# Kernel optimization log

Measured on AMD Instinct MI355X. Metric: run time of the kernel, lower is better.

The kernel has to match this reference:

```python
import jax, jax.numpy as jnp
import numpy as np

IN_C, OUT_C, K, STRIDE, PAD = 128, 256, 3, 1, 1
B, H, W = 32, 56, 56


def setup_inputs() -> dict:
    key = jax.random.key(0)
    kx, kw = jax.random.split(key)
    x = jax.random.normal(kx, (B, IN_C, H, W), dtype=jnp.float32)
    # He init, matching torch.randn(out_c,in_c,k,k) * (2/(in_c*k*k))**0.5
    Wk = jax.random.normal(kw, (OUT_C, IN_C, K, K), dtype=jnp.float32) * (2.0 / (IN_C * K * K)) ** 0.5
    b = jnp.zeros((OUT_C,), dtype=jnp.float32)
    return {"x": x, "Wk": Wk, "b": b}


def reference(x, Wk, b):
    # Same math as the module's zero-pad + im2col + GEMM pipeline,
    # expressed as a direct convolution (implicit GEMM).
    out = jax.lax.conv_general_dilated(
        x, Wk,
        window_strides=(STRIDE, STRIDE),
        padding=[(PAD, PAD), (PAD, PAD)],
        dimension_numbers=("NCHW", "OIHW", "NCHW"),
    )
    return out + b[None, :, None, None]
```

## Files before the change

kernel.cpp:

```cpp
#include <hip/hip_runtime.h>
#include <hip/hip_bf16.h>

#define IN_C  128
#define OUT_C 256
#define HIMG  56
#define WIMG  56
#define BIMG  32
#define HW    (HIMG * WIMG)
#define KW    1152

#define BM    128
#define TH    4
#define NLOC  224
#define XROWS 6
#define XCOLS 58
#define NPIXT (XROWS * XCOLS)
#define LDK   40

typedef __attribute__((ext_vector_type(8))) short short8;
typedef __attribute__((ext_vector_type(4))) float float4_;

__device__ __forceinline__ unsigned short f32_to_bf16_rne(float f) {
    unsigned u = __builtin_bit_cast(unsigned, f);
    u += 0x7FFFu + ((u >> 16) & 1u);
    return (unsigned short)(u >> 16);
}

__global__ void repack_w(const float* __restrict__ Wk, unsigned short* __restrict__ Wt) {
    int idx = blockIdx.x * 256 + threadIdx.x;
    if (idx >= OUT_C * KW) return;
    int oc  = idx / KW;
    int rem = idx - oc * KW;
    int r   = rem >> 7;
    int ic  = rem & 127;
    Wt[idx] = f32_to_bf16_rne(Wk[oc * KW + ic * 9 + r]);
}

__global__ __launch_bounds__(256, 2) void conv_gemm(
    const float* __restrict__ x, const unsigned short* __restrict__ Wt,
    const float* __restrict__ bias, float* __restrict__ out)
{
    __shared__ short As[BM * LDK];
    __shared__ short Xs[NPIXT * 32];

    const int tid  = threadIdx.x;
    const int lane = tid & 63;
    const int wid  = tid >> 6;
    const int bx   = blockIdx.x;
    const int b    = bx / 14;
    const int h0   = (bx - b * 14) * TH;
    const int oc0  = blockIdx.y * BM;

    const int wm = (wid >> 1) * 64;
    const int wn = (wid & 1) * 112;

    int lp0[7], outoff[7];
    #pragma unroll
    for (int ni = 0; ni < 7; ++ni) {
        int nl  = wn + ni * 16 + (lane & 15);
        int ht_ = nl / 56;
        int wt_ = nl - ht_ * 56;
        lp0[ni]    = (ht_ + 1) * XCOLS + (wt_ + 1);
        outoff[ni] = (h0 + ht_) * WIMG + wt_;
    }

    const short* aptr[4];
    #pragma unroll
    for (int mi = 0; mi < 4; ++mi)
        aptr[mi] = &As[(wm + mi * 16 + (lane & 15)) * LDK + (lane >> 4) * 8];

    float4_ acc[4][7];
    #pragma unroll
    for (int mi = 0; mi < 4; ++mi)
        #pragma unroll
        for (int ni = 0; ni < 7; ++ni) acc[mi][ni] = (float4_)0.0f;

    const int am = tid >> 1, ako = (tid & 1) * 16;
    const int q  = lane >> 4;

    short8 w0, w1;
    {
        const unsigned short* srcA = Wt + (size_t)(oc0 + am) * KW + 0 * 128 + 0 * 32 + ako;
        w0 = *(const short8*)srcA;
        w1 = *(const short8*)(srcA + 8);
    }

    for (int t = 0; t < 36; ++t) {
        const int icq = t / 9;
        const int r   = t - icq * 9;

        if (r == 0) {
            for (int pix = tid; pix < NPIXT; pix += 256) {
                int row  = pix / XCOLS;
                int colw = pix - row * XCOLS;
                int h = h0 + row - 1;
                int w = colw - 1;
                bool valid = ((unsigned)h < HIMG) & ((unsigned)w < WIMG);
                const int sw = (pix >> 1) & 3;
                #pragma unroll
                for (int qb = 0; qb < 4; ++qb) {
                    const float* src = x + (size_t)(b * IN_C + icq * 32 + qb * 8) * HW
                                         + (ptrdiff_t)(h * WIMG + w);
                    short8 v;
                    #pragma unroll
                    for (int j = 0; j < 8; ++j) {
                        float f = valid ? src[(size_t)j * HW] : 0.0f;
                        v[j] = (short)f32_to_bf16_rne(f);
                    }
                    *(short8*)&Xs[pix * 32 + (qb ^ sw) * 8] = v;
                }
            }
        }

        *(short8*)&As[am * LDK + ako]     = w0;
        *(short8*)&As[am * LDK + ako + 8] = w1;
        if (t < 35) {
            const int t1   = t + 1;
            const int icq1 = t1 / 9;
            const int r1   = t1 - icq1 * 9;
            const unsigned short* srcA =
                Wt + (size_t)(oc0 + am) * KW + r1 * 128 + icq1 * 32 + ako;
            w0 = *(const short8*)srcA;
            w1 = *(const short8*)(srcA + 8);
        }
        __syncthreads();

        const int doff = (r / 3 - 1) * XCOLS + (r - (r / 3) * 3 - 1);
        short8 afr[4], bfr[7];
        #pragma unroll
        for (int mi = 0; mi < 4; ++mi) afr[mi] = *(const short8*)aptr[mi];
        #pragma unroll
        for (int ni = 0; ni < 7; ++ni) {
            int lp   = lp0[ni] + doff;
            int slot = q ^ ((lp >> 1) & 3);
            bfr[ni]  = *(const short8*)&Xs[lp * 32 + slot * 8];
        }
        #pragma unroll
        for (int mi = 0; mi < 4; ++mi)
            #pragma unroll
            for (int ni = 0; ni < 7; ++ni)
                acc[mi][ni] = __builtin_amdgcn_mfma_f32_16x16x32_bf16(
                    afr[mi], bfr[ni], acc[mi][ni], 0, 0, 0);
        __syncthreads();
    }

    const int rowg = (lane >> 4) * 4;
    #pragma unroll
    for (int mi = 0; mi < 4; ++mi) {
        #pragma unroll
        for (int v = 0; v < 4; ++v) {
            const int oc = oc0 + wm + mi * 16 + rowg + v;
            const float bv = bias[oc];
            float* obase = out + (size_t)(b * OUT_C + oc) * HW;
            #pragma unroll
            for (int ni = 0; ni < 7; ++ni)
                obase[outoff[ni]] = acc[mi][ni][v] + bv;
        }
    }
}

extern "C" void kernel_launch(void* const* d_in, const int* in_sizes, int n_in,
                              void* d_out, int out_size, void* d_ws, size_t ws_size,
                              hipStream_t stream) {
    const float* x    = (const float*)d_in[0];
    const float* Wk   = (const float*)d_in[1];
    const float* bias = (const float*)d_in[2];
    float* out        = (float*)d_out;
    unsigned short* Wt = (unsigned short*)d_ws;

    repack_w<<<dim3((OUT_C * KW + 255) / 256), dim3(256), 0, stream>>>(Wk, Wt);
    conv_gemm<<<dim3(BIMG * (HIMG / TH), OUT_C / BM), dim3(256), 0, stream>>>(x, Wt, bias, out);
}
```

Measured before the change: 214.6 us.

## Pre-pack input to padded NHWC bf16 and async-pipeline LDS tiles

Adds a pre-pass that converts x into a zero-padded NHWC bf16 buffer and repacks the weights into pre-swizzled per-step tiles. The GEMM kernel then fills LDS directly with global_load_lds async copies: a 4-deep ring buffer for weight tiles and a double buffer for input tiles. It waits with manual vmcnt counts and a single barrier per step, and raises wave priority around the MFMA block. This removes the in-kernel strided fp32 gathers, conversions and the second barrier. It costs an extra transpose kernel, extra workspace traffic and more LDS, which may reduce occupancy.

Result: faster. 201.1 us (-6.3%).

```diff
diff --git a/kernel.cpp b/kernel.cpp
--- a/kernel.cpp
+++ b/kernel.cpp
@@ -1,5 +1,4 @@
 #include <hip/hip_runtime.h>
-#include <hip/hip_bf16.h>
 
 #define IN_C  128
 #define OUT_C 256
@@ -11,11 +10,16 @@
 
 #define BM    128
 #define TH    4
-#define NLOC  224
 #define XROWS 6
 #define XCOLS 58
 #define NPIXT (XROWS * XCOLS)
-#define LDK   40
+#define XS_SH (NPIXT * 32)
+#define AS_SH 4096
+#define NT    36
+#define WT_TILES 39
+#define XCH   (NPIXT * 4)
+
+#define NX_BYTES 27557888u
 
 typedef __attribute__((ext_vector_type(8))) short short8;
 typedef __attribute__((ext_vector_type(4))) float float4_;
@@ -26,22 +30,61 @@
     return (unsigned short)(u >> 16);
 }
 
+#define ASYNC16(g, l) __builtin_amdgcn_global_load_lds( \
+    (const __attribute__((address_space(1))) unsigned int*)(g), \
+    (__attribute__((address_space(3))) unsigned int*)(l), 16, 0, 0)
+
+__global__ __launch_bounds__(256) void x_to_nhwc(
+    const float* __restrict__ x, unsigned short* __restrict__ nx)
+{
+    __shared__ unsigned short T[128][58];
+    const int b  = blockIdx.x;
+    const int hp = blockIdx.y;
+    unsigned short* dst = nx + (size_t)(b * 58 + hp) * 58 * 128;
+
+    if (hp == 0 || hp == 57) {
+        for (int i = threadIdx.x; i < 58 * 128; i += 256) dst[i] = 0;
+        return;
+    }
+    const int h = hp - 1;
+    for (int e = threadIdx.x; e < 128 * 56; e += 256) {
+        int c = e / 56, w = e - c * 56;
+        T[c][w] = f32_to_bf16_rne(x[(size_t)(b * IN_C + c) * HW + h * WIMG + w]);
+    }
+    __syncthreads();
+    for (int e = threadIdx.x; e < 58 * 128; e += 256) {
+        int wp = e >> 7, c = e & 127;
+        dst[wp * 128 + c] = (wp == 0 || wp == 57) ? (unsigned short)0 : T[c][wp - 1];
+    }
+}
+
 __global__ void repack_w(const float* __restrict__ Wk, unsigned short* __restrict__ Wt) {
     int idx = blockIdx.x * 256 + threadIdx.x;
-    if (idx >= OUT_C * KW) return;
-    int oc  = idx / KW;
-    int rem = idx - oc * KW;
-    int r   = rem >> 7;
-    int ic  = rem & 127;
-    Wt[idx] = f32_to_bf16_rne(Wk[oc * KW + ic * 9 + r]);
+    if (idx >= 2 * WT_TILES * 4096) return;
+    int half = idx / (WT_TILES * 4096);
+    int rem  = idx - half * (WT_TILES * 4096);
+    int t    = rem >> 12;
+    int win  = rem & 4095;
+    int oc   = win >> 5;
+    int c    = (win >> 3) & 3;
+    int j    = win & 7;
+    unsigned short v = 0;
+    if (t < NT) {
+        int icq = t / 9, r = t - icq * 9;
+        int s  = c ^ ((oc >> 1) & 3);
+        int ic = icq * 32 + s * 8 + j;
+        v = f32_to_bf16_rne(Wk[(size_t)(half * 128 + oc) * KW + ic * 9 + r]);
+    }
+    Wt[idx] = v;
 }
 
 __global__ __launch_bounds__(256, 2) void conv_gemm(
-    const float* __restrict__ x, const unsigned short* __restrict__ Wt,
+    const unsigned short* __restrict__ nx,
+    const unsigned short* __restrict__ Wt,
     const float* __restrict__ bias, float* __restrict__ out)
 {
-    __shared__ short As[BM * LDK];
-    __shared__ short Xs[NPIXT * 32];
+    __shared__ __align__(16) unsigned short As[4 * AS_SH];
+    __shared__ __align__(16) unsigned short Xs[2 * XS_SH];
 
     const int tid  = threadIdx.x;
     const int lane = tid & 63;
@@ -49,10 +92,11 @@
     const int bx   = blockIdx.x;
     const int b    = bx / 14;
     const int h0   = (bx - b * 14) * TH;
-    const int oc0  = blockIdx.y * BM;
+    const int half = blockIdx.y;
 
     const int wm = (wid >> 1) * 64;
     const int wn = (wid & 1) * 112;
+    const int q  = lane >> 4;
 
     int lp0[7], outoff[7];
     #pragma unroll
@@ -64,87 +108,91 @@
         outoff[ni] = (h0 + ht_) * WIMG + wt_;
     }
 
-    const short* aptr[4];
+    int aoff[4];
+    #pragma unroll
+    for (int mi = 0; mi < 4; ++mi) {
+        int row = wm + mi * 16 + (lane & 15);
+        aoff[mi] = row * 32 + ((q ^ ((row >> 1) & 3)) * 8);
+    }
+
+    int xgo[6];
+    #pragma unroll
+    for (int i = 0; i < 6; ++i) {
+        int C = wid * 348 + i * 64 + lane;
+        if (C >= XCH) C = XCH - 1;
+        int p = C >> 2, c = C & 3;
+        int row  = p / XCOLS;
+        int colw = p - row * XCOLS;
+        int s = c ^ ((p >> 1) & 3);
+        xgo[i] = ((b * 58 + h0 + row) * 58 + colw) * 256 + s * 16;
+    }
+    const char* nxc = (const char*)nx;
+    const char* wtc = (const char*)Wt + (size_t)half * WT_TILES * 8192
+                    + (wid * 2) * 1024 + lane * 16;
+
+    float4_ acc[4][7];
     #pragma unroll
     for (int mi = 0; mi < 4; ++mi)
-        aptr[mi] = &As[(wm + mi * 16 + (lane & 15)) * LDK + (lane >> 4) * 8];
-
-    float4_ acc[4][7];
-    #pragma unroll
-    for (int mi = 0; mi < 4; ++mi)
         #pragma unroll
         for (int ni = 0; ni < 7; ++ni) acc[mi][ni] = (float4_)0.0f;
 
-    const int am = tid >> 1, ako = (tid & 1) * 16;
-    const int q  = lane >> 4;
-
-    short8 w0, w1;
-    {
-        const unsigned short* srcA = Wt + (size_t)(oc0 + am) * KW + 0 * 128 + 0 * 32 + ako;
-        w0 = *(const short8*)srcA;
-        w1 = *(const short8*)(srcA + 8);
-    }
-
-    for (int t = 0; t < 36; ++t) {
+    auto stage_x = [&](int icq1, int bufX1) {
+        #pragma unroll
+        for (int i = 0; i < 5; ++i)
+            ASYNC16(nxc + xgo[i] + icq1 * 64,
+                    &Xs[bufX1 * XS_SH + (wid * 348 + i * 64) * 8]);
+        if (lane < 28)
+            ASYNC16(nxc + xgo[5] + icq1 * 64,
+                    &Xs[bufX1 * XS_SH + (wid * 348 + 5 * 64) * 8]);
+    };
+    auto stage_a = [&](int tile) {
+        const char* src = wtc + (size_t)tile * 8192;
+        unsigned short* dst = &As[(tile & 3) * AS_SH + (wid * 2) * 512];
+        ASYNC16(src, dst);
+        ASYNC16(src + 1024, dst + 512);
+    };
+
+    stage_x(0, 0);
+    stage_a(0); stage_a(1); stage_a(2);
+
+    for (int t = 0; t < NT; ++t) {
         const int icq = t / 9;
         const int r   = t - icq * 9;
 
-        if (r == 0) {
-            for (int pix = tid; pix < NPIXT; pix += 256) {
-                int row  = pix / XCOLS;
-                int colw = pix - row * XCOLS;
-                int h = h0 + row - 1;
-                int w = colw - 1;
-                bool valid = ((unsigned)h < HIMG) & ((unsigned)w < WIMG);
-                const int sw = (pix >> 1) & 3;
-                #pragma unroll
-                for (int qb = 0; qb < 4; ++qb) {
-                    const float* src = x + (size_t)(b * IN_C + icq * 32 + qb * 8) * HW
-                                         + (ptrdiff_t)(h * WIMG + w);
-                    short8 v;
-                    #pragma unroll
-                    for (int j = 0; j < 8; ++j) {
-                        float f = valid ? src[(size_t)j * HW] : 0.0f;
-                        v[j] = (short)f32_to_bf16_rne(f);
-                    }
-                    *(short8*)&Xs[pix * 32 + (qb ^ sw) * 8] = v;
-                }
-            }
-        }
-
-        *(short8*)&As[am * LDK + ako]     = w0;
-        *(short8*)&As[am * LDK + ako + 8] = w1;
-        if (t < 35) {
-            const int t1   = t + 1;
-            const int icq1 = t1 / 9;
-            const int r1   = t1 - icq1 * 9;
-            const unsigned short* srcA =
-                Wt + (size_t)(oc0 + am) * KW + r1 * 128 + icq1 * 32 + ako;
-            w0 = *(const short8*)srcA;
-            w1 = *(const short8*)(srcA + 8);
-        }
-        __syncthreads();
-
+        if (r >= 1 && r <= 3) asm volatile("s_waitcnt vmcnt(10)" ::: "memory");
+        else                  asm volatile("s_waitcnt vmcnt(4)"  ::: "memory");
+        __builtin_amdgcn_s_barrier();
+        asm volatile("" ::: "memory");
+
+        const unsigned short* Ab = &As[(t & 3) * AS_SH];
+        const unsigned short* Xb = &Xs[(icq & 1) * XS_SH];
         const int doff = (r / 3 - 1) * XCOLS + (r - (r / 3) * 3 - 1);
+
         short8 afr[4], bfr[7];
         #pragma unroll
-        for (int mi = 0; mi < 4; ++mi) afr[mi] = *(const short8*)aptr[mi];
+        for (int mi = 0; mi < 4; ++mi) afr[mi] = *(const short8*)&Ab[aoff[mi]];
         #pragma unroll
         for (int ni = 0; ni < 7; ++ni) {
             int lp   = lp0[ni] + doff;
             int slot = q ^ ((lp >> 1) & 3);
-            bfr[ni]  = *(const short8*)&Xs[lp * 32 + slot * 8];
+            bfr[ni]  = *(const short8*)&Xb[lp * 32 + slot * 8];
         }
+
+        stage_a(t + 3);
+        if (r == 0) stage_x(icq + 1, (icq + 1) & 1);
+
+        __builtin_amdgcn_s_setprio(1);
         #pragma unroll
         for (int mi = 0; mi < 4; ++mi)
             #pragma unroll
             for (int ni = 0; ni < 7; ++ni)
                 acc[mi][ni] = __builtin_amdgcn_mfma_f32_16x16x32_bf16(
                     afr[mi], bfr[ni], acc[mi][ni], 0, 0, 0);
-        __syncthreads();
+        __builtin_amdgcn_s_setprio(0);
     }
 
     const int rowg = (lane >> 4) * 4;
+    const int oc0  = half * BM;
     #pragma unroll
     for (int mi = 0; mi < 4; ++mi) {
         #pragma unroll
@@ -162,12 +210,16 @@
 extern "C" void kernel_launch(void* const* d_in, const int* in_sizes, int n_in,
                               void* d_out, int out_size, void* d_ws, size_t ws_size,
                               hipStream_t stream) {
+    (void)in_sizes; (void)n_in; (void)out_size; (void)ws_size;
     const float* x    = (const float*)d_in[0];
     const float* Wk   = (const float*)d_in[1];
     const float* bias = (const float*)d_in[2];
     float* out        = (float*)d_out;
-    unsigned short* Wt = (unsigned short*)d_ws;
-
-    repack_w<<<dim3((OUT_C * KW + 255) / 256), dim3(256), 0, stream>>>(Wk, Wt);
-    conv_gemm<<<dim3(BIMG * (HIMG / TH), OUT_C / BM), dim3(256), 0, stream>>>(x, Wt, bias, out);
-}
+
+    unsigned short* nx = (unsigned short*)d_ws;
+    unsigned short* Wt = (unsigned short*)((char*)d_ws + NX_BYTES);
+
+    x_to_nhwc<<<dim3(BIMG, 58), dim3(256), 0, stream>>>(x, nx);
+    repack_w<<<dim3((2 * WT_TILES * 4096 + 255) / 256), dim3(256), 0, stream>>>(Wk, Wt);
+    conv_gemm<<<dim3(BIMG * (HIMG / TH), OUT_C / BM), dim3(256), 0, stream>>>(nx, Wt, bias, out);
+}
```
